# Optimization experiments

Measured on AMD Instinct MI355X. Metric: run time of the kernel, lower is better.

## Reference

```python
import jax, jax.numpy as jnp
import numpy as np

B, T, C = 2, 1024, 1024
H = 16
HS = C // H          # head size = 64
ROT = HS // 2        # partial rotary dims = 32
CTX = 1024           # ctx_len (T <= CTX)
FFN_H = 3 * 1024     # GeGLU hidden = 3 * n_ffn
LN_EPS = 1e-5


def setup_inputs():
    key = jax.random.key(0)
    ks = jax.random.split(key, 20)
    s = 0.02
    f32 = jnp.float32
    p = {}
    p["x"] = jax.random.normal(ks[0], (B, T, C), f32)
    p["ln1_w"] = jnp.ones((C,), f32); p["ln1_b"] = jnp.zeros((C,), f32)
    p["ln2_w"] = jnp.ones((C,), f32); p["ln2_b"] = jnp.zeros((C,), f32)
    p["Wq"] = jax.random.normal(ks[1], (C, C), f32) * s; p["bq"] = jnp.zeros((C,), f32)
    p["Wk"] = jax.random.normal(ks[2], (C, C), f32) * s; p["bk"] = jnp.zeros((C,), f32)
    p["Wv"] = jax.random.normal(ks[3], (C, C), f32) * s; p["bv"] = jnp.zeros((C,), f32)
    p["Wo"] = jax.random.normal(ks[4], (C, C), f32) * s; p["bo"] = jnp.zeros((C,), f32)
    p["time_w"] = 1.0 + 0.01 * jax.random.normal(ks[5], (H, CTX), f32)
    p["time_alpha"] = 1.0 + 0.01 * jax.random.normal(ks[6], (H, 1, CTX), f32)
    p["time_beta"] = 1.0 + 0.01 * jax.random.normal(ks[7], (H, CTX, 1), f32)
    p["time_gamma"] = 1.0 + 0.01 * jax.random.normal(ks[8], (CTX, 1), f32)
    p["mix_w"] = jnp.eye(H, dtype=f32) + 0.02 * jax.random.normal(ks[9], (H, H), f32)
    p["Wkg"] = jax.random.normal(ks[10], (C, FFN_H), f32) * s; p["bkg"] = jnp.zeros((FFN_H,), f32)
    p["Wvg"] = jax.random.normal(ks[11], (C, FFN_H), f32) * s; p["bvg"] = jnp.zeros((FFN_H,), f32)
    p["Wwg"] = jax.random.normal(ks[12], (FFN_H, C), f32) * s; p["bwg"] = jnp.zeros((C,), f32)
    return p


def _ln(x, w, b):
    m = jnp.mean(x, axis=-1, keepdims=True)
    v = jnp.mean((x - m) ** 2, axis=-1, keepdims=True)
    return (x - m) * jax.lax.rsqrt(v + LN_EPS) * w + b


def _time_shift_half(x):
    # ZeroPad2d((0,0,1,-1)) on the first C//2 channels: shift down by one step in time
    c = x.shape[-1]
    shifted = jnp.pad(x[:, :-1, : c // 2], ((0, 0), (1, 0), (0, 0)))
    return jnp.concatenate([shifted, x[:, :, c // 2 :]], axis=-1)


def _decay_w(time_w, time_alpha, time_beta):
    # Toeplitz trick: [H, CTX] -> circulant [H, CTX, CTX] of relative-time weights
    TT = CTX
    w = jnp.pad(time_w, ((0, 0), (0, TT)))                 # [H, 2TT]
    w = jnp.tile(w, (1, TT))[:, :-TT]                      # [H, 2TT*TT - TT]
    w = w.reshape(-1, TT, 2 * TT - 1)[:, :, TT - 1 :]      # [H, TT, TT]
    return w[:, :T, :T] * time_alpha[:, :, :T] * time_beta[:, :T, :]


def _rotate_half(x):
    x1, x2 = x[..., : x.shape[-1] // 2], x[..., x.shape[-1] // 2 :]
    return jnp.concatenate([-x2, x1], axis=-1)


def _apply_rotary(q, k):
    # q, k: [B, H, T, ROT]
    inv_freq = 1.0 / (10000.0 ** (jnp.arange(0, ROT, 2, dtype=jnp.float32) / ROT))
    t = jnp.arange(T, dtype=jnp.float32)
    freqs = t[:, None] * inv_freq[None, :]                 # [T, ROT//2]
    emb = jnp.concatenate([freqs, freqs], axis=-1)         # [T, ROT]
    cos, sin = jnp.cos(emb), jnp.sin(emb)
    q = q * cos + _rotate_half(q) * sin
    k = k * cos + _rotate_half(k) * sin
    return q, k


def _mha_pro(x, Wq, bq, Wk, bk, Wv, bv, Wo, bo,
             time_w, time_alpha, time_beta, time_gamma, mix_w):
    w = _decay_w(time_w, time_alpha, time_beta)            # [H, T, T]
    xs = _time_shift_half(x)
    q = (xs @ Wq + bq).reshape(B, T, H, HS).transpose(0, 2, 1, 3)
    k = (xs @ Wk + bk).reshape(B, T, H, HS).transpose(0, 2, 1, 3)
    v = (xs @ Wv + bv).reshape(B, T, H, HS).transpose(0, 2, 1, 3)
    qr, qp = q[..., :ROT], q[..., ROT:]
    kr, kp = k[..., :ROT], k[..., ROT:]
    qr, kr = _apply_rotary(qr, kr)
    q = jnp.concatenate([qr, qp], axis=-1)
    k = jnp.concatenate([kr, kp], axis=-1)
    att = jnp.einsum('bhqd,bhkd->bhqk', q, k) * (1.0 / np.sqrt(HS))
    causal = jnp.tril(jnp.ones((T, T), dtype=bool))
    att = jnp.where(causal, att, -jnp.inf)
    att = jax.nn.softmax(att, axis=-1)
    att = att * w                                          # learned time-decay reweighting
    att = jnp.einsum('oi,biqk->boqk', mix_w, att)          # 1x1 conv head mixing
    y = jnp.einsum('bhqk,bhkd->bhqd', att, v)
    y = y.transpose(0, 2, 1, 3).reshape(B, T, C)
    return (y @ Wo + bo) * time_gamma[:T, :]


def _geglu(x, Wkg, bkg, Wvg, bvg, Wwg, bwg):
    kk = x @ Wkg + bkg
    vv = x @ Wvg + bvg
    return (jax.nn.gelu(kk, approximate=False) * vv) @ Wwg + bwg


def _block(x, ln1_w, ln1_b, ln2_w, ln2_b, Wq, bq, Wk, bk, Wv, bv, Wo, bo,
           time_w, time_alpha, time_beta, time_gamma, mix_w,
           Wkg, bkg, Wvg, bvg, Wwg, bwg):
    x = x + _mha_pro(_ln(x, ln1_w, ln1_b), Wq, bq, Wk, bk, Wv, bv, Wo, bo,
                     time_w, time_alpha, time_beta, time_gamma, mix_w)
    x = x + _geglu(_ln(x, ln2_w, ln2_b), Wkg, bkg, Wvg, bvg, Wwg, bwg)
    return x


def reference(x, ln1_w, ln1_b, ln2_w, ln2_b, Wq, bq, Wk, bk, Wv, bv, Wo, bo,
              time_w, time_alpha, time_beta, time_gamma, mix_w,
              Wkg, bkg, Wvg, bvg, Wwg, bwg):
    return _block(x, ln1_w, ln1_b, ln2_w, ln2_b, Wq, bq, Wk, bk, Wv, bv, Wo, bo,
                  time_w, time_alpha, time_beta, time_gamma, mix_w,
                  Wkg, bkg, Wvg, bvg, Wwg, bwg)
```

## Files before the change

### kernel.cpp

```cpp
#include <hip/hip_runtime.h>
#include <cstdint>
#include <cstddef>
#include <cstdio>

#define B_   2
#define T_   1024
#define C_   1024
#define H_   16
#define HS_  64
#define FFN_ 3072

typedef __bf16   bf16x8 __attribute__((ext_vector_type(8)));
typedef float    f32x4  __attribute__((ext_vector_type(4)));
typedef float    f32x16 __attribute__((ext_vector_type(16)));
typedef uint16_t u16x8  __attribute__((ext_vector_type(8)));

__device__ __forceinline__ uint16_t f2bf(float f){
  uint32_t u = __float_as_uint(f);
  u += 0x7FFFu + ((u >> 16) & 1u);
  return (uint16_t)(u >> 16);
}
__device__ __forceinline__ float bf2f(uint16_t h){
  return __uint_as_float(((uint32_t)h) << 16);
}
__device__ __forceinline__ bf16x8 ldb8(const uint16_t* p){
  return __builtin_bit_cast(bf16x8, *reinterpret_cast<const u16x8*>(p));
}
__device__ __forceinline__ f32x4 mfma16(bf16x8 a, bf16x8 b, f32x4 c){
  return __builtin_amdgcn_mfma_f32_16x16x32_bf16(a, b, c, 0, 0, 0);
}

typedef __attribute__((address_space(1))) const uint32_t* gas_t;
typedef __attribute__((address_space(3))) uint32_t* las_t;
__device__ __forceinline__ void gl_lds16(const uint16_t* g, uint16_t* l){
  __builtin_amdgcn_global_load_lds((gas_t)g, (las_t)l, 16, 0, 0);
}

__global__ __launch_bounds__(256) void k_transpose(const float* __restrict__ in,
                                                   uint16_t* __restrict__ out,
                                                   int R, int Cc){
  __shared__ float tile[32][33];
  int c0 = blockIdx.x*32, r0 = blockIdx.y*32;
  int tx = threadIdx.x, ty = threadIdx.y;
  #pragma unroll
  for (int i=0;i<4;i++) tile[ty+i*8][tx] = in[(size_t)(r0+ty+i*8)*Cc + c0+tx];
  __syncthreads();
  #pragma unroll
  for (int i=0;i<4;i++) out[(size_t)(c0+ty+i*8)*R + r0+tx] = f2bf(tile[tx][ty+i*8]);
}

__global__ void k_bcat(const float* __restrict__ bq, const float* __restrict__ bk,
                       const float* __restrict__ bv, const float* __restrict__ bkg,
                       const float* __restrict__ bvg, float* __restrict__ out){
  int i = blockIdx.x*256 + threadIdx.x;
  float v;
  if      (i < 1024) v = bq[i];
  else if (i < 2048) v = bk[i-1024];
  else if (i < 3072) v = bv[i-2048];
  else if (i < 6144) v = bkg[i-3072];
  else               v = bvg[i-6144];
  out[i] = v;
}

template<int SHIFT>
__global__ __launch_bounds__(256) void k_ln(const float* __restrict__ in,
                                            const float* __restrict__ w,
                                            const float* __restrict__ bia,
                                            uint16_t* __restrict__ out){
  int row = blockIdx.x;
  int t = row & (T_-1);
  const float* xr = in + (size_t)row*C_;
  float4 v = reinterpret_cast<const float4*>(xr)[threadIdx.x];
  float s  = v.x+v.y+v.z+v.w;
  float s2 = v.x*v.x+v.y*v.y+v.z*v.z+v.w*v.w;
  #pragma unroll
  for (int o=1;o<64;o<<=1){ s += __shfl_xor(s,o); s2 += __shfl_xor(s2,o); }
  __shared__ float red[8];
  int lane = threadIdx.x & 63, wid = threadIdx.x >> 6;
  if (lane == 0){ red[wid] = s; red[4+wid] = s2; }
  __syncthreads();
  s  = red[0]+red[1]+red[2]+red[3];
  s2 = red[4]+red[5]+red[6]+red[7];
  float mean = s * (1.f/1024.f);
  float var  = s2 * (1.f/1024.f) - mean*mean;
  float rs   = rsqrtf(var + 1e-5f);
  float vals[4] = {v.x, v.y, v.z, v.w};
  #pragma unroll
  for (int j=0;j<4;j++){
    int cc = threadIdx.x*4 + j;
    float o_ = (vals[j]-mean)*rs*w[cc] + bia[cc];
    uint16_t ob = f2bf(o_);
    if (SHIFT){
      if (cc < 512){
        if (t < T_-1) out[(size_t)(row+1)*C_ + cc] = ob;
        if (t == 0)   out[(size_t)row*C_ + cc] = 0;
      } else {
        out[(size_t)row*C_ + cc] = ob;
      }
    } else {
      out[(size_t)row*C_ + cc] = ob;
    }
  }
}

enum { EPI_QKV=0, EPI_WO=2, EPI_BF16=3, EPI_FFN2=4 };

template<int EPI, int BN>
__global__ __launch_bounds__(256) void k_gemm2(
    const uint16_t* __restrict__ A, const uint16_t* __restrict__ Bt,
    const float* __restrict__ bias, void* __restrict__ outp,
    int M, int N, int K,
    const float* __restrict__ aux0, const float* __restrict__ aux1)
{
  __shared__ uint16_t As[128*32];
  __shared__ uint16_t Bs[BN*32];
  const int m0 = blockIdx.y*128, n0 = blockIdx.x*BN;
  const int tid = threadIdx.x;
  const int lane = tid & 63, wid = tid >> 6;
  const int wy = wid >> 1, wx = wid & 1;
  const int l16 = lane & 15, lr = lane >> 4;
  const int WN = BN/2;
  const int NW = BN/32;
  const f32x4 z = {0.f,0.f,0.f,0.f};
  f32x4 acc[4][NW];
  #pragma unroll
  for (int m=0;m<4;m++)
    #pragma unroll
    for (int n=0;n<NW;n++) acc[m][n] = z;
  const int srow = tid >> 2, scol = (tid & 3)*8;
  for (int k0 = 0; k0 < K; k0 += 32){
    gl_lds16(A + (size_t)(m0 + srow)*K      + k0 + scol, As + tid*8);
    gl_lds16(A + (size_t)(m0 + 64 + srow)*K + k0 + scol, As + 2048 + tid*8);
    gl_lds16(Bt + (size_t)(n0 + srow)*K     + k0 + scol, Bs + tid*8);
    if constexpr (BN == 128)
      gl_lds16(Bt + (size_t)(n0 + 64 + srow)*K + k0 + scol, Bs + 2048 + tid*8);
    __syncthreads();
    bf16x8 af[4], bfr[NW];
    #pragma unroll
    for (int m=0;m<4;m++) af[m] = ldb8(As + (wy*64 + m*16 + l16)*32 + lr*8);
    #pragma unroll
    for (int n=0;n<NW;n++) bfr[n] = ldb8(Bs + (wx*WN + n*16 + l16)*32 + lr*8);
    #pragma unroll
    for (int m=0;m<4;m++)
      #pragma unroll
      for (int n=0;n<NW;n++) acc[m][n] = mfma16(af[m], bfr[n], acc[m][n]);
    __syncthreads();
  }
  if constexpr (EPI == EPI_QKV){
    const int colb = n0 + wx*WN;
    const int kind = colb >> 10;
    const int h = (colb >> 6) & 15;
    const float linvf = exp2f(-(float)l16 * 0.83048202f);
    #pragma unroll
    for (int m=0;m<4;m++){
      #pragma unroll
      for (int r=0;r<4;r++){
        int row = m0 + wy*64 + m*16 + lr*4 + r;
        int bb = row >> 10, t = row & 1023;
        float v[NW];
        #pragma unroll
        for (int n=0;n<NW;n++) v[n] = acc[m][n][r] + bias[colb + n*16 + l16];
        if (kind < 2){
          float sn, cs;
          __sincosf((float)t * linvf, &sn, &cs);
          float r0 = v[0]*cs - v[1]*sn;
          float r1 = v[1]*cs + v[0]*sn;
          v[0] = r0; v[1] = r1;
          uint16_t* dst = (uint16_t*)outp + (size_t)kind*2097152;
          size_t basei = (((size_t)bb*16 + h)*1024 + t)*64;
          #pragma unroll
          for (int n=0;n<NW;n++) dst[basei + n*16 + l16] = f2bf(v[n]);
        } else {
          uint16_t* dst = (uint16_t*)outp + (size_t)2*2097152;
          size_t basei = ((size_t)bb*16 + h)*65536;
          #pragma unroll
          for (int n=0;n<NW;n++) dst[basei + (size_t)(n*16 + l16)*1024 + t] = f2bf(v[n]);
        }
      }
    }
  } else {
    #pragma unroll
    for (int m=0;m<4;m++){
      #pragma unroll
      for (int n=0;n<NW;n++){
        int col = n0 + wx*WN + n*16 + l16;
        float bc_ = bias ? bias[col] : 0.f;
        #pragma unroll
        for (int r=0;r<4;r++){
          int row = m0 + wy*64 + m*16 + lr*4 + r;
          float v = acc[m][n][r] + bc_;
          if constexpr (EPI == EPI_WO){
            int t = row & (T_-1);
            ((float*)outp)[(size_t)row*N + col] = aux1[(size_t)row*N + col] + v*aux0[t];
          } else if constexpr (EPI == EPI_BF16){
            ((uint16_t*)outp)[(size_t)row*N + col] = f2bf(v);
          } else {
            ((float*)outp)[(size_t)row*N + col] = aux0[(size_t)row*N + col] + v;
          }
        }
      }
    }
  }
}

__global__ __launch_bounds__(256) void k_stats(const uint16_t* __restrict__ q,
                                               const uint16_t* __restrict__ kmat,
                                               float* __restrict__ sm, float* __restrict__ sl){
  int bh = blockIdx.x, qb = blockIdx.y;
  int lane = threadIdx.x & 63, wid = threadIdx.x >> 6;
  int l16 = lane & 15, lr = lane >> 4;
  int r0 = qb*64 + wid*16;
  const uint16_t* qh = q    + (size_t)bh*T_*HS_;
  const uint16_t* kh = kmat + (size_t)bh*T_*HS_;
  int kq = lr*8;
  bf16x8 a0 = ldb8(qh + (size_t)(r0 + l16)*HS_ + kq);
  bf16x8 a1 = ldb8(qh + (size_t)(r0 + l16)*HS_ + kq + 32);
  float m_[4], l_[4]; int rows[4];
  #pragma unroll
  for (int r=0;r<4;r++){ m_[r] = -1e30f; l_[r] = 0.f; rows[r] = r0 + lr*4 + r; }
  int ktmax = (r0 + 15) >> 4;
  for (int kt = 0; kt <= ktmax; kt++){
    bf16x8 b0 = ldb8(kh + (size_t)(kt*16 + l16)*HS_ + kq);
    bf16x8 b1 = ldb8(kh + (size_t)(kt*16 + l16)*HS_ + kq + 32);
    f32x4 s = {0.f,0.f,0.f,0.f};
    s = mfma16(a0, b0, s);
    s = mfma16(a1, b1, s);
    int kcol = kt*16 + l16;
    #pragma unroll
    for (int r=0;r<4;r++){
      float sv = (kcol <= rows[r]) ? s[r]*0.125f : -3.0e38f;
      float mn = fmaxf(m_[r], sv);
      l_[r] = l_[r]*__expf(m_[r] - mn) + __expf(sv - mn);
      m_[r] = mn;
    }
  }
  #pragma unroll
  for (int o=1;o<16;o<<=1){
    #pragma unroll
    for (int r=0;r<4;r++){
      float mo = __shfl_xor(m_[r], o);
      float lo = __shfl_xor(l_[r], o);
      float mn = fmaxf(m_[r], mo);
      l_[r] = l_[r]*__expf(m_[r] - mn) + lo*__expf(mo - mn);
      m_[r] = mn;
    }
  }
  if (l16 == 0){
    #pragma unroll
    for (int r=0;r<4;r++){
      sm[(size_t)bh*T_ + rows[r]] = m_[r];
      sl[(size_t)bh*T_ + rows[r]] = l_[r];
    }
  }
}

__global__ __launch_bounds__(512, 2) void k_attn(
    const uint16_t* __restrict__ q, const uint16_t* __restrict__ kmat,
    const uint16_t* __restrict__ vT,
    const float* __restrict__ sm, const float* __restrict__ sl,
    const float* __restrict__ tw, const float* __restrict__ alpha,
    const float* __restrict__ beta, const float* __restrict__ mixw,
    uint16_t* __restrict__ py)
{
  int qt = blockIdx.x, kc = blockIdx.y, b = blockIdx.z;
  if (8*kc > qt) return;
  const int q0 = qt*16, ck0 = kc*128;
  const int lc = min(127, q0 + 15 - ck0);
  const int nt = (lc >> 5) + 1;

  __shared__ uint32_t U32[2*4096];
  __shared__ uint16_t Cm[2*8320];
  __shared__ uint16_t TWL[16*160];

  const int tid = threadIdx.x;
  const int lane = tid & 63;
  const int wid = __builtin_amdgcn_readfirstlane(tid >> 6);
  const int l16 = lane & 15, lr = lane >> 4;
  const int l32 = lane & 31, g32 = lane >> 5;

  const int base = 1008 - q0 + ck0;
  for (int i = tid; i < 16*144; i += 512){
    int h = i / 144, t = i - h*144;
    int gi = base + t;
    TWL[h*160 + t] = (gi <= 1023) ? f2bf(tw[h*1024 + gi]) : (uint16_t)0;
  }

  float SM[2][4], BSL[2][4];
  bf16x8 qa[2][2];
  #pragma unroll
  for (int h2=0; h2<2; ++h2){
    int h = 2*wid + h2, bh = b*16 + h;
    float4 s4 = *reinterpret_cast<const float4*>(sm   + (size_t)bh*1024 + q0 + lr*4);
    float4 l4 = *reinterpret_cast<const float4*>(sl   + (size_t)bh*1024 + q0 + lr*4);
    float4 b4 = *reinterpret_cast<const float4*>(beta + (size_t)h*1024  + q0 + lr*4);
    SM[h2][0]=s4.x; SM[h2][1]=s4.y; SM[h2][2]=s4.z; SM[h2][3]=s4.w;
    BSL[h2][0]=b4.x/l4.x; BSL[h2][1]=b4.y/l4.y; BSL[h2][2]=b4.z/l4.z; BSL[h2][3]=b4.w/l4.w;
    #pragma unroll
    for (int kk=0;kk<2;kk++)
      qa[h2][kk] = ldb8(q + ((size_t)bh*1024 + q0 + l16)*64 + kk*32 + lr*8);
  }
  bf16x8 mwf;
  {
    u16x8 t8;
    #pragma unroll
    for (int j=0;j<8;j++){
      float v = (l32 < 16) ? mixw[l32*16 + g32*8 + j] : 0.f;
      t8[j] = f2bf(v);
    }
    mwf = __builtin_bit_cast(bf16x8, t8);
  }

  const f32x4 z = {0.f,0.f,0.f,0.f};
  f32x4 acc[2][4];
  #pragma unroll
  for (int oo=0;oo<2;oo++) for (int n=0;n<4;n++) acc[oo][n] = z;

  __syncthreads();

  for (int tp = 0; tp < nt; tp += 2){
    const int ntile = (nt - tp >= 2) ? 2 : 1;
    #pragma unroll
    for (int half = 0; half < 2; ++half){
      if (half >= ntile) break;
      const int t = tp + half;
      const int k0 = ck0 + t*32;
      float al0[2], al1[2];
      #pragma unroll
      for (int n=0;n<2;n++){
        int kg = k0 + n*16 + l16;
        al0[n] = alpha[(2*wid+0)*1024 + kg];
        al1[n] = alpha[(2*wid+1)*1024 + kg];
      }
      f32x4 s[2][2];
      s[0][0]=z; s[0][1]=z; s[1][0]=z; s[1][1]=z;
      #pragma unroll
      for (int h2=0;h2<2;h2++){
        const uint16_t* kh = kmat + ((size_t)(b*16 + 2*wid + h2)*1024 + k0)*64;
        #pragma unroll
        for (int kk=0;kk<2;kk++){
          bf16x8 kb0 = ldb8(kh + (size_t)(l16)*64      + kk*32 + lr*8);
          bf16x8 kb1 = ldb8(kh + (size_t)(16 + l16)*64 + kk*32 + lr*8);
          s[h2][0] = mfma16(qa[h2][kk], kb0, s[h2][0]);
          s[h2][1] = mfma16(qa[h2][kk], kb1, s[h2][1]);
        }
      }
      uint32_t* Ub = U32 + half*4096;
      #pragma unroll
      for (int n=0;n<2;n++){
        int kloc = n*16 + l16;
        int kg = k0 + kloc;
        #pragma unroll
        for (int r=0;r<4;r++){
          int qloc = lr*4 + r;
          bool ok = (kg <= q0 + qloc);
          int twi = 15 - qloc + (kg - ck0);
          float u0 = 0.f, u1 = 0.f;
          if (ok){
            u0 = __expf(s[0][n][r]*0.125f - SM[0][r]) * BSL[0][r] * al0[n] * bf2f(TWL[(2*wid+0)*160 + twi]);
            u1 = __expf(s[1][n][r]*0.125f - SM[1][r]) * BSL[1][r] * al1[n] * bf2f(TWL[(2*wid+1)*160 + twi]);
          }
          uint32_t pk = (uint32_t)f2bf(u0) | ((uint32_t)f2bf(u1) << 16);
          Ub[wid*512 + qloc*32 + ((kloc + 8*(qloc>>2)) & 31)] = pk;
        }
      }
    }
    __syncthreads();
    #pragma unroll
    for (int half = 0; half < 2; ++half){
      if (half >= ntile) break;
      const uint32_t* Ub = U32 + half*4096;
      uint16_t* Cb = Cm + half*8320;
      #pragma unroll
      for (int cc=0; cc<2; ++cc){
        int qrow = wid*2 + cc;
        int pbase = qrow*32;
        int swz = (l32 + 8*(qrow>>2)) & 31;
        u16x8 a8;
        uint32_t* a32 = reinterpret_cast<uint32_t*>(&a8);
        #pragma unroll
        for (int j=0;j<4;j++)
          a32[j] = Ub[(4*g32 + j)*512 + pbase + swz];
        bf16x8 a = __builtin_bit_cast(bf16x8, a8);
        f32x16 zz{};
        __builtin_amdgcn_s_setprio(1);
        f32x16 dd = __builtin_amdgcn_mfma_f32_32x32x16_bf16(a, mwf, zz, 0, 0, 0);
        __builtin_amdgcn_s_setprio(0);
        if (l32 < 16){
          int o = l32;
          #pragma unroll
          for (int rg=0; rg<4; ++rg){
            int p0 = pbase + rg*8 + g32*4;
            uint32_t w0 = (uint32_t)f2bf(dd[4*rg+0]) | ((uint32_t)f2bf(dd[4*rg+1]) << 16);
            uint32_t w1 = (uint32_t)f2bf(dd[4*rg+2]) | ((uint32_t)f2bf(dd[4*rg+3]) << 16);
            uint2 pk2; pk2.x = w0; pk2.y = w1;
            *reinterpret_cast<uint2*>(Cb + (size_t)o*520 + p0) = pk2;
          }
        }
      }
    }
    __syncthreads();
    #pragma unroll
    for (int half = 0; half < 2; ++half){
      if (half >= ntile) break;
      const int k0 = ck0 + (tp + half)*32;
      const uint16_t* Cb = Cm + half*8320;
      #pragma unroll
      for (int oo=0;oo<2;oo++){
        int o = 2*wid + oo;
        bf16x8 cf = ldb8(Cb + (size_t)o*520 + l16*32 + lr*8);
        const uint16_t* vh = vT + (size_t)(b*16 + o)*65536;
        __builtin_amdgcn_s_setprio(1);
        #pragma unroll
        for (int n=0;n<4;n++){
          bf16x8 vf = ldb8(vh + (size_t)(n*16 + l16)*1024 + k0 + lr*8);
          acc[oo][n] = mfma16(cf, vf, acc[oo][n]);
        }
        __builtin_amdgcn_s_setprio(0);
      }
    }
  }

  uint16_t* po = py + (((size_t)(b*64 + qt))*8 + kc)*16384;
  #pragma unroll
  for (int oo=0;oo<2;oo++){
    int o = 2*wid + oo;
    #pragma unroll
    for (int n=0;n<4;n++)
      #pragma unroll
      for (int r=0;r<4;r++){
        int qloc = lr*4 + r;
        po[o*1024 + qloc*64 + n*16 + l16] = f2bf(acc[oo][n][r]);
      }
  }
}

__global__ void k_yred(const uint16_t* __restrict__ py, uint16_t* __restrict__ y){
  int idx = blockIdx.x*256 + threadIdx.x;
  int d8 = idx & 7, qq = (idx>>3)&15, o = (idx>>7)&15, qt = (idx>>11)&63, b = idx>>17;
  int nch = (qt>>3) + 1;
  const uint16_t* p0 = py + (((size_t)(b*64+qt))*8)*16384 + o*1024 + qq*64 + d8*8;
  float s[8] = {0,0,0,0,0,0,0,0};
  for (int kc=0; kc<nch; kc++){
    u16x8 v = *reinterpret_cast<const u16x8*>(p0 + (size_t)kc*16384);
    #pragma unroll
    for (int e=0;e<8;e++) s[e] += bf2f(v[e]);
  }
  int t = qt*16 + qq;
  u16x8 w;
  #pragma unroll
  for (int e=0;e<8;e++) w[e] = f2bf(s[e]);
  *reinterpret_cast<u16x8*>(y + ((size_t)(b*1024 + t))*1024 + o*64 + d8*8) = w;
}

__global__ void k_geglu(const uint16_t* __restrict__ ffu, uint16_t* __restrict__ g){
  int i = blockIdx.x*256 + threadIdx.x;
  int row = i / 384, j8 = i - row*384;
  const uint16_t* pa = ffu + (size_t)row*6144 + j8*8;
  u16x8 a = *reinterpret_cast<const u16x8*>(pa);
  u16x8 b = *reinterpret_cast<const u16x8*>(pa + 3072);
  u16x8 o;
  #pragma unroll
  for (int e=0;e<8;e++){
    float xv = bf2f(a[e]);
    float gl = 0.5f*xv*(1.f + erff(xv*0.70710678118f));
    o[e] = f2bf(gl * bf2f(b[e]));
  }
  *reinterpret_cast<u16x8*>(g + (size_t)row*3072 + j8*8) = o;
}

extern "C" void kernel_launch(void* const* d_in, const int* in_sizes, int n_in,
                              void* d_out, int out_size, void* d_ws, size_t ws_size,
                              hipStream_t stream)
{
  const float* x      = (const float*)d_in[0];
  const float* ln1w   = (const float*)d_in[1];
  const float* ln1b   = (const float*)d_in[2];
  const float* ln2w   = (const float*)d_in[3];
  const float* ln2b   = (const float*)d_in[4];
  const float* Wq     = (const float*)d_in[5];
  const float* bq     = (const float*)d_in[6];
  const float* Wk     = (const float*)d_in[7];
  const float* bk     = (const float*)d_in[8];
  const float* Wv     = (const float*)d_in[9];
  const float* bv     = (const float*)d_in[10];
  const float* Wo     = (const float*)d_in[11];
  const float* bo     = (const float*)d_in[12];
  const float* tw     = (const float*)d_in[13];
  const float* talpha = (const float*)d_in[14];
  const float* tbeta  = (const float*)d_in[15];
  const float* tgamma = (const float*)d_in[16];
  const float* mixw   = (const float*)d_in[17];
  const float* Wkg    = (const float*)d_in[18];
  const float* bkg    = (const float*)d_in[19];
  const float* Wvg    = (const float*)d_in[20];
  const float* bvg    = (const float*)d_in[21];
  const float* Wwg    = (const float*)d_in[22];
  const float* bwg    = (const float*)d_in[23];

  char* ws = (char*)d_ws;
  size_t off = 0;
  auto alloc = [&](size_t bytes)->char*{
    char* p = ws + off; off += (bytes + 255) & ~(size_t)255; return p;
  };
  uint16_t* WqT  = (uint16_t*)alloc((size_t)C_*C_*2);
  uint16_t* WkT  = (uint16_t*)alloc((size_t)C_*C_*2);
  uint16_t* WvT  = (uint16_t*)alloc((size_t)C_*C_*2);
  uint16_t* WoT  = (uint16_t*)alloc((size_t)C_*C_*2);
  uint16_t* WkgT = (uint16_t*)alloc((size_t)FFN_*C_*2);
  uint16_t* WvgT = (uint16_t*)alloc((size_t)FFN_*C_*2);
  uint16_t* WwgT = (uint16_t*)alloc((size_t)C_*FFN_*2);
  uint16_t* xs   = (uint16_t*)alloc((size_t)B_*T_*C_*2);
  uint16_t* qbuf = (uint16_t*)alloc((size_t)B_*T_*C_*2);
  uint16_t* kbuf = (uint16_t*)alloc((size_t)B_*T_*C_*2);
  uint16_t* vT   = (uint16_t*)alloc((size_t)B_*T_*C_*2);
  float*    sm   = (float*)alloc((size_t)B_*H_*T_*4);
  float*    sl   = (float*)alloc((size_t)B_*H_*T_*4);
  uint16_t* ybuf = (uint16_t*)alloc((size_t)B_*T_*C_*2);
  float*    x1   = (float*)alloc((size_t)B_*T_*C_*4);
  float*    bcat = (float*)alloc((size_t)9216*4);
  char*     region = alloc((size_t)64*1024*1024);
  uint16_t* py  = (uint16_t*)region;
  uint16_t* ffu = (uint16_t*)region;
  uint16_t* gb  = (uint16_t*)(region + (size_t)2048*6144*2);

  if (off > ws_size){
    fprintf(stderr, "kernel_launch: ws too small (%zu needed, %zu given)\n", off, ws_size);
    return;
  }

  dim3 blk(256);
  dim3 tblk(32,8);
  k_transpose<<<dim3(32,32), tblk, 0, stream>>>(Wq,  WqT,  C_,  C_);
  k_transpose<<<dim3(32,32), tblk, 0, stream>>>(Wk,  WkT,  C_,  C_);
  k_transpose<<<dim3(32,32), tblk, 0, stream>>>(Wv,  WvT,  C_,  C_);
  k_transpose<<<dim3(32,32), tblk, 0, stream>>>(Wo,  WoT,  C_,  C_);
  k_transpose<<<dim3(96,32), tblk, 0, stream>>>(Wkg, WkgT, C_,  FFN_);
  k_transpose<<<dim3(96,32), tblk, 0, stream>>>(Wvg, WvgT, C_,  FFN_);
  k_transpose<<<dim3(32,96), tblk, 0, stream>>>(Wwg, WwgT, FFN_, C_);
  k_bcat<<<36, blk, 0, stream>>>(bq, bk, bv, bkg, bvg, bcat);

  k_ln<1><<<B_*T_, blk, 0, stream>>>(x, ln1w, ln1b, xs);

  k_gemm2<EPI_QKV,128><<<dim3(24,16), blk, 0, stream>>>(xs, WqT, bcat, qbuf, 2048, 3072, 1024, nullptr, nullptr);

  k_stats<<<dim3(B_*H_, T_/64), blk, 0, stream>>>(qbuf, kbuf, sm, sl);
  k_attn<<<dim3(64,8,B_), dim3(512), 0, stream>>>(qbuf, kbuf, vT, sm, sl,
                                                  tw, talpha, tbeta, mixw, py);
  k_yred<<<1024, blk, 0, stream>>>(py, ybuf);

  k_gemm2<EPI_WO,64><<<dim3(16,16), blk, 0, stream>>>(ybuf, WoT, bo, x1, 2048, 1024, 1024, tgamma, x);

  k_ln<0><<<B_*T_, blk, 0, stream>>>(x1, ln2w, ln2b, xs);

  k_gemm2<EPI_BF16,128><<<dim3(48,16), blk, 0, stream>>>(xs, WkgT, bcat+3072, ffu, 2048, 6144, 1024, nullptr, nullptr);
  k_geglu<<<3072, blk, 0, stream>>>(ffu, gb);
  k_gemm2<EPI_FFN2,64><<<dim3(16,16), blk, 0, stream>>>(gb, WwgT, bwg, d_out, 2048, 1024, 3072, x1, nullptr);
}
```

Baseline: 301.4 us.

## Double-buffer LDS tiles in GEMM to overlap global loads with MFMA

The GEMM kernel now keeps two LDS buffers for the A and B tiles. It issues direct-to-LDS loads for the next K-slice before computing on the current one, and the previous two __syncthreads per iteration become a single waitcnt plus barrier. The goal is to hide global memory latency behind the MFMA work and cut synchronization. The cost is doubled LDS use, which may lower occupancy. There is also a possible hazard: the next-stage writes into the other buffer can race with waves still reading it from the previous iteration, since the only barrier sits after compute.

```diff
diff --git a/kernel.cpp b/kernel.cpp
--- a/kernel.cpp
+++ b/kernel.cpp
@@ -112,8 +112,8 @@
     int M, int N, int K,
     const float* __restrict__ aux0, const float* __restrict__ aux1)
 {
-  __shared__ uint16_t As[128*32];
-  __shared__ uint16_t Bs[BN*32];
+  __shared__ uint16_t As[2][128*32];
+  __shared__ uint16_t Bs[2][BN*32];
   const int m0 = blockIdx.y*128, n0 = blockIdx.x*BN;
   const int tid = threadIdx.x;
   const int lane = tid & 63, wid = tid >> 6;
@@ -128,24 +128,40 @@
     #pragma unroll
     for (int n=0;n<NW;n++) acc[m][n] = z;
   const int srow = tid >> 2, scol = (tid & 3)*8;
+
+  auto STAGE = [&](int buf, int k0){
+    gl_lds16(A + (size_t)(m0 + srow)*K      + k0 + scol, As[buf] + tid*8);
+    gl_lds16(A + (size_t)(m0 + 64 + srow)*K + k0 + scol, As[buf] + 2048 + tid*8);
+    gl_lds16(Bt + (size_t)(n0 + srow)*K     + k0 + scol, Bs[buf] + tid*8);
+    if constexpr (BN == 128)
+      gl_lds16(Bt + (size_t)(n0 + 64 + srow)*K + k0 + scol, Bs[buf] + 2048 + tid*8);
+  };
+
+  STAGE(0, 0);
+  asm volatile("s_waitcnt vmcnt(0)");
+  __builtin_amdgcn_s_barrier();
+
+  int cur = 0;
   for (int k0 = 0; k0 < K; k0 += 32){
-    gl_lds16(A + (size_t)(m0 + srow)*K      + k0 + scol, As + tid*8);
-    gl_lds16(A + (size_t)(m0 + 64 + srow)*K + k0 + scol, As + 2048 + tid*8);
-    gl_lds16(Bt + (size_t)(n0 + srow)*K     + k0 + scol, Bs + tid*8);
-    if constexpr (BN == 128)
-      gl_lds16(Bt + (size_t)(n0 + 64 + srow)*K + k0 + scol, Bs + 2048 + tid*8);
-    __syncthreads();
+    const bool more = (k0 + 32 < K);
+    if (more) STAGE(cur^1, k0 + 32);
     bf16x8 af[4], bfr[NW];
     #pragma unroll
-    for (int m=0;m<4;m++) af[m] = ldb8(As + (wy*64 + m*16 + l16)*32 + lr*8);
-    #pragma unroll
-    for (int n=0;n<NW;n++) bfr[n] = ldb8(Bs + (wx*WN + n*16 + l16)*32 + lr*8);
+    for (int m=0;m<4;m++) af[m] = ldb8(As[cur] + (wy*64 + m*16 + l16)*32 + lr*8);
+    #pragma unroll
+    for (int n=0;n<NW;n++) bfr[n] = ldb8(Bs[cur] + (wx*WN + n*16 + l16)*32 + lr*8);
     #pragma unroll
     for (int m=0;m<4;m++)
       #pragma unroll
       for (int n=0;n<NW;n++) acc[m][n] = mfma16(af[m], bfr[n], acc[m][n]);
-    __syncthreads();
-  }
+    __builtin_amdgcn_sched_barrier(0);
+    if (more){
+      asm volatile("s_waitcnt vmcnt(0)");
+      __builtin_amdgcn_s_barrier();
+    }
+    cur ^= 1;
+  }
+
   if constexpr (EPI == EPI_QKV){
     const int colb = n0 + wx*WN;
     const int kind = colb >> 10;
```

Measured after the change: 349.2 us. 15.9% more time.

## Fuse weight transposes, bias concat and LN1 into one prep kernel; narrow QKV tiles

Applied to the files above, without the earlier changes.

Merges the seven weight-transpose launches, the bias concatenation and the first layernorm into a single k_prep launch that dispatches on block index. This removes launch overhead and serialization gaps between many small kernels. The QKV GEMM switches from 128-wide to 64-wide N tiles, doubling the grid for better CU occupancy, with the rotary epilogue rewritten for the 2-fragment-per-wave layout. The narrower tiles bring more redundant A-tile loads per output.

```diff
diff --git a/kernel.cpp b/kernel.cpp
--- a/kernel.cpp
+++ b/kernel.cpp
@@ -36,30 +36,94 @@
   __builtin_amdgcn_global_load_lds((gas_t)g, (las_t)l, 16, 0, 0);
 }
 
-__global__ __launch_bounds__(256) void k_transpose(const float* __restrict__ in,
-                                                   uint16_t* __restrict__ out,
-                                                   int R, int Cc){
+__global__ __launch_bounds__(256) void k_prep(
+    const float* __restrict__ Wq, const float* __restrict__ Wk,
+    const float* __restrict__ Wv, const float* __restrict__ Wo,
+    const float* __restrict__ Wkg, const float* __restrict__ Wvg,
+    const float* __restrict__ Wwg,
+    const float* __restrict__ bq, const float* __restrict__ bk,
+    const float* __restrict__ bv, const float* __restrict__ bkg,
+    const float* __restrict__ bvg,
+    const float* __restrict__ x, const float* __restrict__ ln1w,
+    const float* __restrict__ ln1b,
+    uint16_t* __restrict__ WqT, uint16_t* __restrict__ WkT,
+    uint16_t* __restrict__ WvT, uint16_t* __restrict__ WoT,
+    uint16_t* __restrict__ WkgT, uint16_t* __restrict__ WvgT,
+    uint16_t* __restrict__ WwgT, float* __restrict__ bcat,
+    uint16_t* __restrict__ xs)
+{
   __shared__ float tile[32][33];
-  int c0 = blockIdx.x*32, r0 = blockIdx.y*32;
-  int tx = threadIdx.x, ty = threadIdx.y;
-  #pragma unroll
-  for (int i=0;i<4;i++) tile[ty+i*8][tx] = in[(size_t)(r0+ty+i*8)*Cc + c0+tx];
-  __syncthreads();
-  #pragma unroll
-  for (int i=0;i<4;i++) out[(size_t)(c0+ty+i*8)*R + r0+tx] = f2bf(tile[tx][ty+i*8]);
-}
-
-__global__ void k_bcat(const float* __restrict__ bq, const float* __restrict__ bk,
-                       const float* __restrict__ bv, const float* __restrict__ bkg,
-                       const float* __restrict__ bvg, float* __restrict__ out){
-  int i = blockIdx.x*256 + threadIdx.x;
-  float v;
-  if      (i < 1024) v = bq[i];
-  else if (i < 2048) v = bk[i-1024];
-  else if (i < 3072) v = bv[i-2048];
-  else if (i < 6144) v = bkg[i-3072];
-  else               v = bvg[i-6144];
-  out[i] = v;
+  __shared__ float red[8];
+  const int id = blockIdx.x;
+  const int tid = threadIdx.x;
+
+  if (id < 13312){
+    const float* in; uint16_t* outp; int R, Cc, bx, by;
+    if (id < 4096){
+      int w = id >> 10, r = id & 1023;
+      in   = (w==0)?Wq:(w==1)?Wk:(w==2)?Wv:Wo;
+      outp = (w==0)?WqT:(w==1)?WkT:(w==2)?WvT:WoT;
+      R = 1024; Cc = 1024; bx = r & 31; by = r >> 5;
+    } else if (id < 10240){
+      int r = id - 4096; int w = r / 3072; r -= w*3072;
+      in = w ? Wvg : Wkg; outp = w ? WvgT : WkgT;
+      R = 1024; Cc = 3072; bx = r % 96; by = r / 96;
+    } else {
+      int r = id - 10240;
+      in = Wwg; outp = WwgT; R = 3072; Cc = 1024;
+      bx = r & 31; by = r >> 5;
+    }
+    int c0 = bx*32, r0 = by*32;
+    int tx = tid & 31, ty = tid >> 5;
+    #pragma unroll
+    for (int i=0;i<4;i++) tile[ty+i*8][tx] = in[(size_t)(r0+ty+i*8)*Cc + c0+tx];
+    __syncthreads();
+    #pragma unroll
+    for (int i=0;i<4;i++) outp[(size_t)(c0+ty+i*8)*R + r0+tx] = f2bf(tile[tx][ty+i*8]);
+    return;
+  }
+  if (id < 13348){
+    int i = (id - 13312)*256 + tid;
+    float v;
+    if      (i < 1024) v = bq[i];
+    else if (i < 2048) v = bk[i-1024];
+    else if (i < 3072) v = bv[i-2048];
+    else if (i < 6144) v = bkg[i-3072];
+    else               v = bvg[i-6144];
+    bcat[i] = v;
+    return;
+  }
+  {
+    int row = id - 13348;
+    int t = row & (T_-1);
+    const float* xr = x + (size_t)row*C_;
+    float4 v = reinterpret_cast<const float4*>(xr)[tid];
+    float s  = v.x+v.y+v.z+v.w;
+    float s2 = v.x*v.x+v.y*v.y+v.z*v.z+v.w*v.w;
+    #pragma unroll
+    for (int o=1;o<64;o<<=1){ s += __shfl_xor(s,o); s2 += __shfl_xor(s2,o); }
+    int lane = tid & 63, wv = tid >> 6;
+    if (lane == 0){ red[wv] = s; red[4+wv] = s2; }
+    __syncthreads();
+    s  = red[0]+red[1]+red[2]+red[3];
+    s2 = red[4]+red[5]+red[6]+red[7];
+    float mean = s * (1.f/1024.f);
+    float var  = s2 * (1.f/1024.f) - mean*mean;
+    float rs   = rsqrtf(var + 1e-5f);
+    float vals[4] = {v.x, v.y, v.z, v.w};
+    #pragma unroll
+    for (int j=0;j<4;j++){
+      int cc = tid*4 + j;
+      float o_ = (vals[j]-mean)*rs*ln1w[cc] + ln1b[cc];
+      uint16_t ob = f2bf(o_);
+      if (cc < 512){
+        if (t < T_-1) xs[(size_t)(row+1)*C_ + cc] = ob;
+        if (t == 0)   xs[(size_t)row*C_ + cc] = 0;
+      } else {
+        xs[(size_t)row*C_ + cc] = ob;
+      }
+    }
+  }
 }
 
 template<int SHIFT>
@@ -147,9 +211,6 @@
     __syncthreads();
   }
   if constexpr (EPI == EPI_QKV){
-    const int colb = n0 + wx*WN;
-    const int kind = colb >> 10;
-    const int h = (colb >> 6) & 15;
     const float linvf = exp2f(-(float)l16 * 0.83048202f);
     #pragma unroll
     for (int m=0;m<4;m++){
@@ -157,24 +218,27 @@
       for (int r=0;r<4;r++){
         int row = m0 + wy*64 + m*16 + lr*4 + r;
         int bb = row >> 10, t = row & 1023;
-        float v[NW];
-        #pragma unroll
-        for (int n=0;n<NW;n++) v[n] = acc[m][n][r] + bias[colb + n*16 + l16];
-        if (kind < 2){
+        int col0 = n0 + wx*32 + l16;
+        float v0 = acc[m][0][r] + bias[col0];
+        float v1 = acc[m][1][r] + bias[col0+16];
+        int kind = col0 >> 10, hcol = col0 & 1023;
+        int h = hcol >> 6, d0 = hcol & 63;
+        if (kind < 2 && wx == 0){
           float sn, cs;
           __sincosf((float)t * linvf, &sn, &cs);
-          float r0 = v[0]*cs - v[1]*sn;
-          float r1 = v[1]*cs + v[0]*sn;
-          v[0] = r0; v[1] = r1;
-          uint16_t* dst = (uint16_t*)outp + (size_t)kind*2097152;
+          float r0 = v0*cs - v1*sn;
+          float r1 = v1*cs + v0*sn;
+          v0 = r0; v1 = r1;
+        }
+        uint16_t* dst = (uint16_t*)outp + (size_t)kind*2097152;
+        if (kind < 2){
           size_t basei = (((size_t)bb*16 + h)*1024 + t)*64;
-          #pragma unroll
-          for (int n=0;n<NW;n++) dst[basei + n*16 + l16] = f2bf(v[n]);
+          dst[basei + d0]      = f2bf(v0);
+          dst[basei + d0 + 16] = f2bf(v1);
         } else {
-          uint16_t* dst = (uint16_t*)outp + (size_t)2*2097152;
           size_t basei = ((size_t)bb*16 + h)*65536;
-          #pragma unroll
-          for (int n=0;n<NW;n++) dst[basei + (size_t)(n*16 + l16)*1024 + t] = f2bf(v[n]);
+          dst[basei + (size_t)d0*1024 + t]      = f2bf(v0);
+          dst[basei + (size_t)(d0+16)*1024 + t] = f2bf(v1);
         }
       }
     }
@@ -529,19 +593,13 @@
   }
 
   dim3 blk(256);
-  dim3 tblk(32,8);
-  k_transpose<<<dim3(32,32), tblk, 0, stream>>>(Wq,  WqT,  C_,  C_);
-  k_transpose<<<dim3(32,32), tblk, 0, stream>>>(Wk,  WkT,  C_,  C_);
-  k_transpose<<<dim3(32,32), tblk, 0, stream>>>(Wv,  WvT,  C_,  C_);
-  k_transpose<<<dim3(32,32), tblk, 0, stream>>>(Wo,  WoT,  C_,  C_);
-  k_transpose<<<dim3(96,32), tblk, 0, stream>>>(Wkg, WkgT, C_,  FFN_);
-  k_transpose<<<dim3(96,32), tblk, 0, stream>>>(Wvg, WvgT, C_,  FFN_);
-  k_transpose<<<dim3(32,96), tblk, 0, stream>>>(Wwg, WwgT, FFN_, C_);
-  k_bcat<<<36, blk, 0, stream>>>(bq, bk, bv, bkg, bvg, bcat);
-
-  k_ln<1><<<B_*T_, blk, 0, stream>>>(x, ln1w, ln1b, xs);
-
-  k_gemm2<EPI_QKV,128><<<dim3(24,16), blk, 0, stream>>>(xs, WqT, bcat, qbuf, 2048, 3072, 1024, nullptr, nullptr);
+  k_prep<<<15396, blk, 0, stream>>>(Wq, Wk, Wv, Wo, Wkg, Wvg, Wwg,
+                                    bq, bk, bv, bkg, bvg,
+                                    x, ln1w, ln1b,
+                                    WqT, WkT, WvT, WoT, WkgT, WvgT, WwgT,
+                                    bcat, xs);
+
+  k_gemm2<EPI_QKV,64><<<dim3(48,16), blk, 0, stream>>>(xs, WqT, bcat, qbuf, 2048, 3072, 1024, nullptr, nullptr);
 
   k_stats<<<dim3(B_*H_, T_/64), blk, 0, stream>>>(qbuf, kbuf, sm, sl);
   k_attn<<<dim3(64,8,B_), dim3(512), 0, stream>>>(qbuf, kbuf, vT, sm, sl,
```

After: 276.7 us. -8.2%, faster.
